# Optimization experiments

Hardware: AMD Instinct MI355X
Metric: run time of the kernel (lower is better)

The kernel has to match this reference:

```python
import jax, jax.numpy as jnp
from jax import lax
import numpy as np

N, K, QK, W = 10, 10, 150, 128
D = 256
HID = 100
CHANS = [1, 16, 32, 64, 128, 256]
STRIDES = [2, 2, 1, 1, 1]
ITERS = 3
BN_EPS = 1e-5


def setup_inputs() -> dict:
    key = jax.random.key(0)
    ks = jax.random.split(key, 12)
    inp = {
        "support": jax.random.normal(ks[0], (N, K, 1, W, W), jnp.float32),
        "query": jax.random.normal(ks[1], (QK, 1, W, W), jnp.float32),
    }
    for i in range(5):
        inp[f"conv_w{i}"] = jax.random.normal(ks[2 + i], (CHANS[i + 1], CHANS[i], 3, 3), jnp.float32) * 0.05
        inp[f"bn_g{i}"] = jnp.ones((CHANS[i + 1],), jnp.float32)
        inp[f"bn_b{i}"] = jnp.zeros((CHANS[i + 1],), jnp.float32)
    inp["trans_w"] = jax.random.normal(ks[8], (D, D), jnp.float32) * 0.05
    inp["trans_b"] = jnp.zeros((D,), jnp.float32)
    inp["bil_w"] = jax.random.normal(ks[9], (HID, D, D), jnp.float32) * 0.02
    inp["score_w"] = jax.random.normal(ks[10], (1, HID), jnp.float32) * 0.1
    inp["score_b"] = jnp.zeros((1,), jnp.float32)
    return inp


def _block(x, w, g, b, s):
    # Conv2d(k=3, pad=1, stride=s, no bias) -> BatchNorm(eval: mean=0, var=1) -> ReLU -> MaxPool2d(2)
    x = lax.conv_general_dilated(x, w, (s, s), ((1, 1), (1, 1)),
                                 dimension_numbers=('NCHW', 'OIHW', 'NCHW'))
    scale = (g / jnp.sqrt(1.0 + BN_EPS))[None, :, None, None]
    x = jax.nn.relu(x * scale + b[None, :, None, None])
    return lax.reduce_window(x, -jnp.inf, lax.max, (1, 1, 2, 2), (1, 1, 2, 2), 'VALID')


def reference(support, query,
              conv_w0, conv_w1, conv_w2, conv_w3, conv_w4,
              bn_g0, bn_g1, bn_g2, bn_g3, bn_g4,
              bn_b0, bn_b1, bn_b2, bn_b3, bn_b4,
              trans_w, trans_b, bil_w, score_w, score_b):
    n, k = support.shape[0], support.shape[1]
    qk = query.shape[0]
    w = support.shape[3]

    ws = [conv_w0, conv_w1, conv_w2, conv_w3, conv_w4]
    gs = [bn_g0, bn_g1, bn_g2, bn_g3, bn_g4]
    bs = [bn_b0, bn_b1, bn_b2, bn_b3, bn_b4]

    # run the conv backbone on support+query jointly (BN is per-sample in eval mode)
    x = jnp.concatenate([support.reshape(n * k, 1, w, w), query], axis=0)
    for cw, g, b, s in zip(ws, gs, bs, STRIDES):
        x = _block(x, cw, g, b, s)
    feats = x.reshape(x.shape[0], -1)              # (n*k + qk, 256); spatial is 1x1
    sup = feats[:n * k].reshape(n, k, -1)          # (n, k, d)
    q = feats[n * k:]                              # (qk, d)

    # dynamic routing: Transformer(e) is recomputed each iter on the same input -> hoist
    e = sup @ trans_w.T + trans_b                  # (n, k, d)
    b0 = jnp.zeros((n, k), sup.dtype)

    def step(bb, _):
        dcoef = jax.nn.softmax(bb, axis=1)[:, :, None]   # (n, k, 1)
        c = (dcoef * e).sum(axis=1)                      # (n, d)
        cn = jnp.sqrt((c * c).sum(axis=1, keepdims=True))
        c = c * (cn / (cn * cn + 1.0))                   # squash: ||c||^2/(||c||^2+1)/||c||
        db = (c[:, None, :] * e).sum(axis=2)             # (n, k)
        return bb + db, c

    _, cs = lax.scan(step, b0, None, length=ITERS)
    proto = cs[-1]                                  # (n, d)

    # NTN: bilinear score for every (query, proto) pair, exploiting the pair structure
    t1 = jnp.einsum('nc,hce->nhe', proto, bil_w)    # (n, HID, d)
    v = jnp.einsum('nhe,qe->qnh', t1, q)            # (qk, n, HID)
    s = jax.nn.relu(v) @ score_w[0] + score_b[0]    # (qk, n)
    return jax.nn.log_softmax(s, axis=1)
```

## Files before the change

### kernel.cpp

```cpp
#include <hip/hip_runtime.h>
#include <math.h>


#define BN_SCALE rsqrtf(1.0f + 1e-5f)

#define OFF_FEATS 0
#define OFF_E     64000
#define OFF_S     89600
#define OFF_T1    91136
#define OFF_PROTO 347136
#define OFF_W1T   349696
#define OFF_W2T   354304
#define OFF_W3T   372736
#define OFF_W4T   446464
#define OFF_TWT   741376
#define OFF_CNT   (OFF_S + 1500)

__global__ void k_prep(const float* __restrict__ w1, const float* __restrict__ w2,
                       const float* __restrict__ w3, const float* __restrict__ w4,
                       const float* __restrict__ tw, float* __restrict__ ws) {
  float* w1t = ws + OFF_W1T;
  float* w2t = ws + OFF_W2T;
  float* w3t = ws + OFF_W3T;
  float* w4t = ws + OFF_W4T;
  float* twt = ws + OFF_TWT;
  int i = blockIdx.x * 256 + threadIdx.x;
  if (i < 4608) {
    int oc = i & 31; int r = i >> 5; int tap = r % 9; int ic = r / 9;
    w1t[i] = w1[(oc * 16 + ic) * 9 + tap];
  } else if (i < 23040) {
    int j = i - 4608;
    int oc = j & 63; int r = j >> 6; int tap = r % 9; int ic = r / 9;
    w2t[j] = w2[(oc * 32 + ic) * 9 + tap];
  } else if (i < 96768) {
    int j = i - 23040;
    int oc = j & 127; int r = j >> 7; int tap = r % 9; int ic = r / 9;
    w3t[j] = w3[(oc * 64 + ic) * 9 + tap];
  } else if (i < 391680) {
    int j = i - 96768;
    int oc = j & 255; int r = j >> 8; int tap = r % 9; int ic = r / 9;
    w4t[j] = w4[(oc * 128 + ic) * 9 + tap];
  } else if (i < 457216) {
    int j = i - 391680;
    int d = j >> 8, c = j & 255;
    twt[j] = tw[c * 256 + d];
  } else if (i < 713216) {
    ws[OFF_T1 + (i - 457216)] = 0.f;
  } else if (i < 714717) {
    ws[OFF_S + (i - 713216)] = 0.f;
  }
}

__global__ void __launch_bounds__(1024, 4)
k_main(const float* __restrict__ sup, const float* __restrict__ qry,
       const float* __restrict__ w0, const float* __restrict__ g0, const float* __restrict__ b0,
       const float* __restrict__ g1, const float* __restrict__ b1,
       const float* __restrict__ g2, const float* __restrict__ b2,
       const float* __restrict__ g3, const float* __restrict__ b3,
       const float* __restrict__ g4, const float* __restrict__ b4,
       const float* __restrict__ tb, float* __restrict__ ws,
       float* __restrict__ feats_g, float* __restrict__ e_buf) {
  __shared__ float S[38404];
  const float* w1t = ws + OFF_W1T;
  const float* w2t = ws + OFF_W2T;
  const float* w3t = ws + OFF_W3T;
  const float* w4t = ws + OFF_W4T;
  const float* twt = ws + OFF_TWT;
  const int img = blockIdx.x;
  const int t = threadIdx.x;
  const int lane = t & 63, wid = t >> 6;
  float* sa1 = S;
  float* sa2 = S + 4096;
  float* sa3 = S + 7424;
  float* sft = S + 7936;
  float* a0p = S + 8580;
  float* RED = S + 8580;
  float* L1R = S + 28164;

  const float* in = (img < 100) ? (sup + (size_t)img * 16384)
                                : (qry + (size_t)(img - 100) * 16384);

  for (int i = t; i < 7424; i += 1024) S[i] = 0.f;
  for (int i = t; i < 19584; i += 1024) a0p[i] = 0.f;
  __syncthreads();

  {
    const int oc = wid;
    float wv[9];
#pragma unroll
    for (int k = 0; k < 9; k++) wv[k] = w0[oc * 9 + k];
    const float sc = g0[oc] * BN_SCALE, bs = b0[oc];
#pragma unroll 2
    for (int it2 = 0; it2 < 4; it2++) {
      const int s2 = it2 * 64 + lane;
      const int pr = s2 >> 3, pcq = s2 & 7;
      float acc[2][8];
#pragma unroll
      for (int j = 0; j < 8; j++) { acc[0][j] = 0.f; acc[1][j] = 0.f; }
#pragma unroll
      for (int d = 0; d < 5; d++) {
        const int ir = 4 * pr - 1 + d;
        float x[17];
        if (ir >= 0) {
          const float* rp = in + ir * 128 + 16 * pcq;
          float4 q0 = ((const float4*)rp)[0];
          float4 q1 = ((const float4*)rp)[1];
          float4 q2 = ((const float4*)rp)[2];
          float4 q3 = ((const float4*)rp)[3];
          x[0] = (pcq > 0) ? rp[-1] : 0.f;
          x[1] = q0.x;  x[2] = q0.y;  x[3] = q0.z;  x[4] = q0.w;
          x[5] = q1.x;  x[6] = q1.y;  x[7] = q1.z;  x[8] = q1.w;
          x[9] = q2.x;  x[10] = q2.y; x[11] = q2.z; x[12] = q2.w;
          x[13] = q3.x; x[14] = q3.y; x[15] = q3.z; x[16] = q3.w;
        } else {
#pragma unroll
          for (int k = 0; k < 17; k++) x[k] = 0.f;
        }
        if (d <= 2) {
          const int b9 = d * 3;
#pragma unroll
          for (int j = 0; j < 8; j++)
            acc[0][j] = fmaf(x[2 * j + 2], wv[b9 + 2],
                        fmaf(x[2 * j + 1], wv[b9 + 1],
                        fmaf(x[2 * j],     wv[b9],     acc[0][j])));
        }
        if (d >= 2) {
          const int b9 = (d - 2) * 3;
#pragma unroll
          for (int j = 0; j < 8; j++)
            acc[1][j] = fmaf(x[2 * j + 2], wv[b9 + 2],
                        fmaf(x[2 * j + 1], wv[b9 + 1],
                        fmaf(x[2 * j],     wv[b9],     acc[1][j])));
        }
      }
      float* op = a0p + oc * 1224 + (pr + 1) * 36 + 4 * pcq + 1;
#pragma unroll
      for (int p = 0; p < 4; p++) {
        float m = fmaf(acc[0][2 * p], sc, bs);
        m = fmaxf(m, fmaf(acc[0][2 * p + 1], sc, bs));
        m = fmaxf(m, fmaf(acc[1][2 * p], sc, bs));
        m = fmaxf(m, fmaf(acc[1][2 * p + 1], sc, bs));
        op[p] = fmaxf(m, 0.f);
      }
    }
  }
  __syncthreads();

  {
    const int pos = t & 63, py = pos >> 3, px = pos & 7;
    const int ocg = (t >> 6) & 7, icg = t >> 9;
    float acc[4][4];
#pragma unroll
    for (int j = 0; j < 4; j++)
#pragma unroll
      for (int p = 0; p < 4; p++) acc[j][p] = 0.f;
    for (int ii = 0; ii < 8; ii++) {
      const int ic = icg * 8 + ii;
      float4 wq[9];
#pragma unroll
      for (int k = 0; k < 9; k++)
        wq[k] = *(const float4*)(w1t + (ic * 9 + k) * 32 + 4 * ocg);
      float win[25];
      const float* bp = a0p + ic * 1224 + 4 * py * 36 + 4 * px;
#pragma unroll
      for (int d = 0; d < 5; d++) {
        float4 r4 = *(const float4*)(bp + d * 36);
        win[d * 5 + 0] = r4.x; win[d * 5 + 1] = r4.y;
        win[d * 5 + 2] = r4.z; win[d * 5 + 3] = r4.w;
        win[d * 5 + 4] = bp[d * 36 + 4];
      }
#pragma unroll
      for (int cy = 0; cy < 2; cy++)
#pragma unroll
        for (int cx = 0; cx < 2; cx++) {
          const int p = cy * 2 + cx;
#pragma unroll
          for (int ky = 0; ky < 3; ky++)
#pragma unroll
            for (int kx = 0; kx < 3; kx++) {
              const float iv = win[(2 * cy + ky) * 5 + (2 * cx + kx)];
              const float4 wk = wq[ky * 3 + kx];
              acc[0][p] = fmaf(iv, wk.x, acc[0][p]);
              acc[1][p] = fmaf(iv, wk.y, acc[1][p]);
              acc[2][p] = fmaf(iv, wk.z, acc[2][p]);
              acc[3][p] = fmaf(iv, wk.w, acc[3][p]);
            }
        }
    }
    const int slot = pos * 8 + ocg;
    if (icg == 1) {
      float* wp2 = L1R + slot * 20;
#pragma unroll
      for (int j = 0; j < 4; j++)
        *(float4*)(wp2 + j * 4) = make_float4(acc[j][0], acc[j][1], acc[j][2], acc[j][3]);
    }
    __syncthreads();
    if (icg == 0) {
      const float* rp2 = L1R + slot * 20;
#pragma unroll
      for (int j = 0; j < 4; j++) {
        float4 o = *(const float4*)(rp2 + j * 4);
        const int oc = ocg * 4 + j;
        const float sc = g1[oc] * BN_SCALE, bsj = b1[oc];
        float m = fmaf(acc[j][0] + o.x, sc, bsj);
        m = fmaxf(m, fmaf(acc[j][1] + o.y, sc, bsj));
        m = fmaxf(m, fmaf(acc[j][2] + o.z, sc, bsj));
        m = fmaxf(m, fmaf(acc[j][3] + o.w, sc, bsj));
        sa1[oc * 124 + (py + 1) * 12 + (px + 1)] = fmaxf(m, 0.f);
      }
    }
  }
  __syncthreads();

  {
    int oc = t & 63, icg = (t >> 6) & 3, pg = t >> 8;
    int pgy = pg >> 1, pgx = pg & 1;
    float acc[16];
#pragma unroll
    for (int p = 0; p < 16; p++) acc[p] = 0.f;
    float wc[9];
    {
      const float* wp = w2t + (icg * 8) * 576 + oc;
#pragma unroll
      for (int k = 0; k < 9; k++) wc[k] = wp[k * 64];
    }
    for (int ii = 0; ii < 8; ii++) {
      int ic = icg * 8 + ii;
      float wn[9];
      if (ii < 7) {
        const float* wp = w2t + (ic + 1) * 576 + oc;
#pragma unroll
        for (int k = 0; k < 9; k++) wn[k] = wp[k * 64];
      }
      float win[6][6];
      const float* bp = sa1 + ic * 124 + 4 * pgy * 12 + 4 * pgx;
#pragma unroll
      for (int d = 0; d < 6; d++) {
        float4 u = *(const float4*)(bp + d * 12);
        float2 v = *(const float2*)(bp + d * 12 + 4);
        win[d][0] = u.x; win[d][1] = u.y; win[d][2] = u.z; win[d][3] = u.w;
        win[d][4] = v.x; win[d][5] = v.y;
      }
#pragma unroll
      for (int u = 0; u < 4; u++)
#pragma unroll
        for (int v = 0; v < 4; v++) {
          float c = acc[u * 4 + v];
#pragma unroll
          for (int ky = 0; ky < 3; ky++)
#pragma unroll
            for (int kx = 0; kx < 3; kx++)
              c = fmaf(win[u + ky][v + kx], wc[ky * 3 + kx], c);
          acc[u * 4 + v] = c;
        }
      if (ii < 7) {
#pragma unroll
        for (int k = 0; k < 9; k++) wc[k] = wn[k];
      }
    }
#pragma unroll
    for (int j = 0; j < 16; j++) RED[j * 1024 + icg * 256 + pg * 64 + oc] = acc[j];
  }
  __syncthreads();
  if (t < 256) {
    int oc = t & 63, pg = t >> 6;
    int pgy = pg >> 1, pgx = pg & 1;
    float sc = g2[oc] * BN_SCALE, bsj = b2[oc];
#pragma unroll
    for (int cy = 0; cy < 2; cy++)
#pragma unroll
      for (int cx = 0; cx < 2; cx++) {
        float m = -1e30f;
#pragma unroll
        for (int a = 0; a < 2; a++)
#pragma unroll
          for (int b = 0; b < 2; b++) {
            int j = (2 * cy + a) * 4 + (2 * cx + b);
            float v = RED[j * 1024 + pg * 64 + oc] + RED[j * 1024 + 256 + pg * 64 + oc]
                    + RED[j * 1024 + 512 + pg * 64 + oc] + RED[j * 1024 + 768 + pg * 64 + oc];
            m = fmaxf(m, fmaf(v, sc, bsj));
          }
        sa2[oc * 52 + (1 + 2 * pgy + cy) * 8 + (1 + 2 * pgx + cx)] = fmaxf(m, 0.f);
      }
  }
  __syncthreads();

  {
    int oc = t & 127, icg = t >> 7;
    float acc[16];
#pragma unroll
    for (int p = 0; p < 16; p++) acc[p] = 0.f;
    float wc[9];
    {
      const float* wp = w3t + (icg * 8) * 1152 + oc;
#pragma unroll
      for (int k = 0; k < 9; k++) wc[k] = wp[k * 128];
    }
    for (int ii = 0; ii < 8; ii++) {
      int ic = icg * 8 + ii;
      float wn[9];
      if (ii < 7) {
        const float* wp = w3t + (ic + 1) * 1152 + oc;
#pragma unroll
        for (int k = 0; k < 9; k++) wn[k] = wp[k * 128];
      }
      float win[6][6];
      const float* bp = sa2 + ic * 52;
#pragma unroll
      for (int d = 0; d < 6; d++) {
        float4 u = *(const float4*)(bp + d * 8);
        float2 v = *(const float2*)(bp + d * 8 + 4);
        win[d][0] = u.x; win[d][1] = u.y; win[d][2] = u.z; win[d][3] = u.w;
        win[d][4] = v.x; win[d][5] = v.y;
      }
#pragma unroll
      for (int u = 0; u < 4; u++)
#pragma unroll
        for (int v = 0; v < 4; v++) {
          float c = acc[u * 4 + v];
#pragma unroll
          for (int ky = 0; ky < 3; ky++)
#pragma unroll
            for (int kx = 0; kx < 3; kx++)
              c = fmaf(win[u + ky][v + kx], wc[ky * 3 + kx], c);
          acc[u * 4 + v] = c;
        }
      if (ii < 7) {
#pragma unroll
        for (int k = 0; k < 9; k++) wc[k] = wn[k];
      }
    }
#pragma unroll
    for (int j = 0; j < 16; j++) RED[j * 1024 + icg * 128 + oc] = acc[j];
  }
  __syncthreads();
  if (t < 512) {
    int oc = t & 127, pp = t >> 7;
    int py = pp >> 1, px = pp & 1;
    float sc = g3[oc] * BN_SCALE, bsj = b3[oc];
    float m = -1e30f;
#pragma unroll
    for (int a = 0; a < 2; a++)
#pragma unroll
      for (int b = 0; b < 2; b++) {
        int j = (2 * py + a) * 4 + (2 * px + b);
        float v = 0.f;
#pragma unroll
        for (int g = 0; g < 8; g++) v += RED[j * 1024 + g * 128 + oc];
        m = fmaxf(m, fmaf(v, sc, bsj));
      }
    sa3[oc * 4 + pp] = fmaxf(m, 0.f);
  }
  __syncthreads();

  {
    int oc = t & 255, icq = t >> 8;
    float acc[4] = {0.f, 0.f, 0.f, 0.f};
    float wc[9];
    {
      const float* wp = w4t + (icq * 32) * 2304 + oc;
#pragma unroll
      for (int k = 0; k < 9; k++) wc[k] = wp[k * 256];
    }
    for (int ii = 0; ii < 32; ii++) {
      int ic = icq * 32 + ii;
      float wn[9];
      if (ii < 31) {
        const float* wp = w4t + (ic + 1) * 2304 + oc;
#pragma unroll
        for (int k = 0; k < 9; k++) wn[k] = wp[k * 256];
      }
      float4 iv = *(const float4*)(sa3 + ic * 4);
#pragma unroll
      for (int py = 0; py < 2; py++)
#pragma unroll
        for (int px = 0; px < 2; px++) {
          float c = acc[py * 2 + px];
          c = fmaf(iv.x, wc[(1 - py) * 3 + (1 - px)], c);
          c = fmaf(iv.y, wc[(1 - py) * 3 + (2 - px)], c);
          c = fmaf(iv.z, wc[(2 - py) * 3 + (1 - px)], c);
          c = fmaf(iv.w, wc[(2 - py) * 3 + (2 - px)], c);
          acc[py * 2 + px] = c;
        }
      if (ii < 31) {
#pragma unroll
        for (int k = 0; k < 9; k++) wc[k] = wn[k];
      }
    }
    if (icq) {
#pragma unroll
      for (int p = 0; p < 4; p++) RED[((icq - 1) * 256 + oc) * 4 + p] = acc[p];
    }
    __syncthreads();
    if (icq == 0) {
      float sc = g4[oc] * BN_SCALE, bsj = b4[oc];
      float m = -1e30f;
#pragma unroll
      for (int p = 0; p < 4; p++) {
        float v = acc[p] + RED[oc * 4 + p] + RED[(256 + oc) * 4 + p] + RED[(512 + oc) * 4 + p];
        m = fmaxf(m, fmaf(v, sc, bsj));
      }
      float r = fmaxf(m, 0.f);
      sft[oc] = r;
      feats_g[(size_t)img * 256 + oc] = r;
    }
  }
  __syncthreads();

  if (img < 100) {
    int c = t & 255, dq = t >> 8;
    float acc = 0.f;
    float wv = twt[(dq * 64) * 256 + c];
#pragma unroll 4
    for (int ii = 0; ii < 64; ii++) {
      int d = dq * 64 + ii;
      float wnext = (ii < 63) ? twt[(d + 1) * 256 + c] : 0.f;
      acc = fmaf(sft[d], wv, acc);
      wv = wnext;
    }
    if (dq) RED[(dq - 1) * 256 + c] = acc;
    __syncthreads();
    if (dq == 0)
      e_buf[img * 256 + c] = acc + RED[c] + RED[256 + c] + RED[512 + c] + tb[c];
  }
}

__global__ void k_routing(const float* __restrict__ e, float* __restrict__ proto) {
  int n = blockIdx.x;
  __shared__ float sb[10], sdc[10], red[4], red2[40], sfc[1];
  int t = threadIdx.x;
  int lane = t & 63, wid = t >> 6;
  float ek[10];
#pragma unroll
  for (int k = 0; k < 10; k++) ek[k] = e[n * 2560 + k * 256 + t];
  if (t < 10) sb[t] = 0.f;
  __syncthreads();
  float cd = 0.f;
  for (int iter = 0; iter < 3; iter++) {
    if (t == 0) {
      float mx = sb[0];
      for (int k = 1; k < 10; k++) mx = fmaxf(mx, sb[k]);
      float sum = 0.f;
      for (int k = 0; k < 10; k++) { float ex = expf(sb[k] - mx); sdc[k] = ex; sum += ex; }
      float inv = 1.f / sum;
      for (int k = 0; k < 10; k++) sdc[k] *= inv;
    }
    __syncthreads();
    cd = 0.f;
#pragma unroll
    for (int k = 0; k < 10; k++) cd = fmaf(sdc[k], ek[k], cd);
    float ss = cd * cd;
#pragma unroll
    for (int off = 32; off > 0; off >>= 1) ss += __shfl_down(ss, off, 64);
    if (lane == 0) red[wid] = ss;
    __syncthreads();
    if (t == 0) {
      float tot = red[0] + red[1] + red[2] + red[3];
      sfc[0] = sqrtf(tot) / (tot + 1.f);
    }
    __syncthreads();
    cd *= sfc[0];
    float pr[10];
#pragma unroll
    for (int k = 0; k < 10; k++) pr[k] = cd * ek[k];
#pragma unroll
    for (int off = 32; off > 0; off >>= 1)
#pragma unroll
      for (int k = 0; k < 10; k++) pr[k] += __shfl_down(pr[k], off, 64);
    if (lane == 0)
#pragma unroll
      for (int k = 0; k < 10; k++) red2[k * 4 + wid] = pr[k];
    __syncthreads();
    if (t < 10) sb[t] += red2[t * 4] + red2[t * 4 + 1] + red2[t * 4 + 2] + red2[t * 4 + 3];
    __syncthreads();
  }
  proto[n * 256 + t] = cd;
}

__global__ void k_t1(const float* __restrict__ proto, const float* __restrict__ bw,
                     float* __restrict__ t1) {
  __shared__ float pt[384];
  const int b = blockIdx.x;
  const int h = b >> 3, c0 = (b & 7) * 32;
  const int t = threadIdx.x;
  for (int i = t; i < 320; i += 256) {
    int n = i >> 5, cl = i & 31;
    pt[cl * 12 + n] = proto[n * 256 + c0 + cl];
  }
  __syncthreads();
  float acc[10];
#pragma unroll
  for (int n = 0; n < 10; n++) acc[n] = 0.f;
  const float* wp = bw + (size_t)h * 65536 + (size_t)c0 * 256 + t;
#pragma unroll 8
  for (int cl = 0; cl < 32; cl++) {
    float wv = wp[(size_t)cl * 256];
    float4 p0 = *(const float4*)(pt + cl * 12);
    float4 p1 = *(const float4*)(pt + cl * 12 + 4);
    float2 p2 = *(const float2*)(pt + cl * 12 + 8);
    acc[0] = fmaf(p0.x, wv, acc[0]); acc[1] = fmaf(p0.y, wv, acc[1]);
    acc[2] = fmaf(p0.z, wv, acc[2]); acc[3] = fmaf(p0.w, wv, acc[3]);
    acc[4] = fmaf(p1.x, wv, acc[4]); acc[5] = fmaf(p1.y, wv, acc[5]);
    acc[6] = fmaf(p1.z, wv, acc[6]); acc[7] = fmaf(p1.w, wv, acc[7]);
    acc[8] = fmaf(p2.x, wv, acc[8]); acc[9] = fmaf(p2.y, wv, acc[9]);
  }
#pragma unroll
  for (int n = 0; n < 10; n++)
    atomicAdd(&t1[((size_t)n * 100 + h) * 256 + t], acc[n]);
}

__global__ void k_score(const float* __restrict__ t1, const float* __restrict__ qf,
                        const float* __restrict__ sw, const float* __restrict__ sbp,
                        float* __restrict__ s, unsigned* __restrict__ cnt,
                        float* __restrict__ out) {
  __shared__ float sq[256];
  __shared__ float vb[2000];
  __shared__ int lastFlag;
  const int q = blockIdx.x >> 1, hh = blockIdx.x & 1;
  const int t = threadIdx.x;
  const int sl = t & 3, quad = t >> 2;
  sq[t] = qf[q * 256 + t];
  __syncthreads();
  const float4* qr = (const float4*)sq;
#pragma unroll
  for (int j = 0; j < 8; j++) {
    int lr = quad + 64 * j;
    if (lr < 500) {
      int n = lr / 50, hl = lr % 50;
      const float4* row = (const float4*)(t1 + ((size_t)(n * 100 + hh * 50 + hl)) * 256);
      float acc = 0.f;
#pragma unroll
      for (int d = 0; d < 16; d++) {
        float4 a = row[d * 4 + sl];
        float4 b = qr[d * 4 + sl];
        acc += a.x * b.x + a.y * b.y + a.z * b.z + a.w * b.w;
      }
      vb[lr * 4 + sl] = acc;
    }
  }
  __syncthreads();
  if (t < 10) {
    float sum = 0.f;
    for (int hl = 0; hl < 50; hl++) {
      int lr = t * 50 + hl;
      float d = vb[lr * 4] + vb[lr * 4 + 1] + vb[lr * 4 + 2] + vb[lr * 4 + 3];
      sum = fmaf(fmaxf(d, 0.f), sw[hh * 50 + hl], sum);
    }
    atomicAdd(&s[q * 10 + t], sum);
    __threadfence();
  }
  __syncthreads();
  if (t == 0) {
    unsigned old = atomicAdd(cnt, 1u);
    lastFlag = (old == 299u);
  }
  __syncthreads();
  if (lastFlag && t < 150) {
    float sb0 = sbp[0];
    float v[10];
    float mx = -1e30f;
#pragma unroll
    for (int n = 0; n < 10; n++) {
      v[n] = atomicAdd(&s[t * 10 + n], 0.f) + sb0;
      mx = fmaxf(mx, v[n]);
    }
    float sum2 = 0.f;
#pragma unroll
    for (int n = 0; n < 10; n++) sum2 += expf(v[n] - mx);
    float lse = mx + logf(sum2);
#pragma unroll
    for (int n = 0; n < 10; n++) out[t * 10 + n] = v[n] - lse;
  }
}

extern "C" void kernel_launch(void* const* d_in, const int* in_sizes, int n_in,
                              void* d_out, int out_size, void* d_ws, size_t ws_size,
                              hipStream_t stream) {
  const float* support = (const float*)d_in[0];
  const float* query   = (const float*)d_in[1];
  const float* conv_w[5]; const float* bn_g[5]; const float* bn_b[5];
  for (int i = 0; i < 5; i++) {
    conv_w[i] = (const float*)d_in[2 + 3 * i];
    bn_g[i]   = (const float*)d_in[3 + 3 * i];
    bn_b[i]   = (const float*)d_in[4 + 3 * i];
  }
  const float* trans_w = (const float*)d_in[17];
  const float* trans_b = (const float*)d_in[18];
  const float* bil_w   = (const float*)d_in[19];
  const float* score_w = (const float*)d_in[20];
  const float* score_b = (const float*)d_in[21];
  float* out = (float*)d_out;
  float* ws = (float*)d_ws;

  float* feats = ws + OFF_FEATS;
  float* e_buf = ws + OFF_E;
  float* s_buf = ws + OFF_S;
  float* t1    = ws + OFF_T1;
  float* proto = ws + OFF_PROTO;
  unsigned* cnt = (unsigned*)(ws + OFF_CNT);

  k_prep<<<2793, 256, 0, stream>>>(conv_w[1], conv_w[2], conv_w[3], conv_w[4],
                                   trans_w, ws);
  k_main<<<250, 1024, 0, stream>>>(support, query,
                                   conv_w[0], bn_g[0], bn_b[0],
                                   bn_g[1], bn_b[1], bn_g[2], bn_b[2],
                                   bn_g[3], bn_b[3], bn_g[4], bn_b[4],
                                   trans_b, ws, feats, e_buf);
  k_routing<<<10, 256, 0, stream>>>(e_buf, proto);
  k_t1<<<800, 256, 0, stream>>>(proto, bil_w, t1);
  k_score<<<300, 256, 0, stream>>>(t1, feats + 100 * 256, score_w, score_b,
                                   s_buf, cnt, out);
}
```

Before: 224.2 us.

## Rework conv0 thread mapping, vectorize shared stores, split log-softmax into own kernel

Layer 0 now gives each warp two output channels over half the rows, so each input load is reused across two channels, and results go out as float4 shared stores. The padded layout shifts so the layer-1 window read becomes one scalar plus one aligned float4. The shared zero-init is merged into a single float4 loop, and the reduction slot order changes. The last-block atomic counter in k_score is replaced by a separate tiny log-softmax kernel, which adds a launch but removes the atomics and fences. The unroll factor in k_t1 also drops from 8 to 4.

```diff
diff --git a/kernel.cpp b/kernel.cpp
--- a/kernel.cpp
+++ b/kernel.cpp
@@ -14,7 +14,6 @@
 #define OFF_W3T   372736
 #define OFF_W4T   446464
 #define OFF_TWT   741376
-#define OFF_CNT   (OFF_S + 1500)
 
 __global__ void k_prep(const float* __restrict__ w1, const float* __restrict__ w2,
                        const float* __restrict__ w3, const float* __restrict__ w4,
@@ -46,7 +45,7 @@
     twt[j] = tw[c * 256 + d];
   } else if (i < 713216) {
     ws[OFF_T1 + (i - 457216)] = 0.f;
-  } else if (i < 714717) {
+  } else if (i < 714716) {
     ws[OFF_S + (i - 713216)] = 0.f;
   }
 }
@@ -60,7 +59,7 @@
        const float* __restrict__ g4, const float* __restrict__ b4,
        const float* __restrict__ tb, float* __restrict__ ws,
        float* __restrict__ feats_g, float* __restrict__ e_buf) {
-  __shared__ float S[38404];
+  __shared__ __align__(16) float S[38404];
   const float* w1t = ws + OFF_W1T;
   const float* w2t = ws + OFF_W2T;
   const float* w3t = ws + OFF_W3T;
@@ -80,23 +79,31 @@
   const float* in = (img < 100) ? (sup + (size_t)img * 16384)
                                 : (qry + (size_t)(img - 100) * 16384);
 
-  for (int i = t; i < 7424; i += 1024) S[i] = 0.f;
-  for (int i = t; i < 19584; i += 1024) a0p[i] = 0.f;
-  __syncthreads();
-
   {
-    const int oc = wid;
-    float wv[9];
-#pragma unroll
-    for (int k = 0; k < 9; k++) wv[k] = w0[oc * 9 + k];
-    const float sc = g0[oc] * BN_SCALE, bs = b0[oc];
-#pragma unroll 2
-    for (int it2 = 0; it2 < 4; it2++) {
-      const int s2 = it2 * 64 + lane;
+    float4* S4 = (float4*)S;
+    const float4 z4 = make_float4(0.f, 0.f, 0.f, 0.f);
+    for (int i = t; i < 7041; i += 1024) S4[i] = z4;
+  }
+  __syncthreads();
+
+  {
+    const int ocp = wid & 7;
+    const int rhalf = wid >> 3;
+    const int oc0 = 2 * ocp, oc1 = oc0 + 1;
+    float wv0[9], wv1[9];
+#pragma unroll
+    for (int k = 0; k < 9; k++) { wv0[k] = w0[oc0 * 9 + k]; wv1[k] = w0[oc1 * 9 + k]; }
+    const float sc0 = g0[oc0] * BN_SCALE, bs0 = b0[oc0];
+    const float sc1 = g0[oc1] * BN_SCALE, bs1 = b0[oc1];
+#pragma unroll
+    for (int it2 = 0; it2 < 2; it2++) {
+      const int s2 = rhalf * 128 + it2 * 64 + lane;
       const int pr = s2 >> 3, pcq = s2 & 7;
-      float acc[2][8];
-#pragma unroll
-      for (int j = 0; j < 8; j++) { acc[0][j] = 0.f; acc[1][j] = 0.f; }
+      float ac0[2][8], ac1[2][8];
+#pragma unroll
+      for (int j = 0; j < 8; j++) {
+        ac0[0][j] = 0.f; ac0[1][j] = 0.f; ac1[0][j] = 0.f; ac1[1][j] = 0.f;
+      }
 #pragma unroll
       for (int d = 0; d < 5; d++) {
         const int ir = 4 * pr - 1 + d;
@@ -119,28 +126,50 @@
         if (d <= 2) {
           const int b9 = d * 3;
 #pragma unroll
-          for (int j = 0; j < 8; j++)
-            acc[0][j] = fmaf(x[2 * j + 2], wv[b9 + 2],
-                        fmaf(x[2 * j + 1], wv[b9 + 1],
-                        fmaf(x[2 * j],     wv[b9],     acc[0][j])));
+          for (int j = 0; j < 8; j++) {
+            ac0[0][j] = fmaf(x[2 * j + 2], wv0[b9 + 2],
+                        fmaf(x[2 * j + 1], wv0[b9 + 1],
+                        fmaf(x[2 * j],     wv0[b9],     ac0[0][j])));
+            ac1[0][j] = fmaf(x[2 * j + 2], wv1[b9 + 2],
+                        fmaf(x[2 * j + 1], wv1[b9 + 1],
+                        fmaf(x[2 * j],     wv1[b9],     ac1[0][j])));
+          }
         }
         if (d >= 2) {
           const int b9 = (d - 2) * 3;
 #pragma unroll
-          for (int j = 0; j < 8; j++)
-            acc[1][j] = fmaf(x[2 * j + 2], wv[b9 + 2],
-                        fmaf(x[2 * j + 1], wv[b9 + 1],
-                        fmaf(x[2 * j],     wv[b9],     acc[1][j])));
-        }
-      }
-      float* op = a0p + oc * 1224 + (pr + 1) * 36 + 4 * pcq + 1;
-#pragma unroll
-      for (int p = 0; p < 4; p++) {
-        float m = fmaf(acc[0][2 * p], sc, bs);
-        m = fmaxf(m, fmaf(acc[0][2 * p + 1], sc, bs));
-        m = fmaxf(m, fmaf(acc[1][2 * p], sc, bs));
-        m = fmaxf(m, fmaf(acc[1][2 * p + 1], sc, bs));
-        op[p] = fmaxf(m, 0.f);
+          for (int j = 0; j < 8; j++) {
+            ac0[1][j] = fmaf(x[2 * j + 2], wv0[b9 + 2],
+                        fmaf(x[2 * j + 1], wv0[b9 + 1],
+                        fmaf(x[2 * j],     wv0[b9],     ac0[1][j])));
+            ac1[1][j] = fmaf(x[2 * j + 2], wv1[b9 + 2],
+                        fmaf(x[2 * j + 1], wv1[b9 + 1],
+                        fmaf(x[2 * j],     wv1[b9],     ac1[1][j])));
+          }
+        }
+      }
+      {
+        float v[4];
+#pragma unroll
+        for (int p = 0; p < 4; p++) {
+          float m = fmaf(ac0[0][2 * p], sc0, bs0);
+          m = fmaxf(m, fmaf(ac0[0][2 * p + 1], sc0, bs0));
+          m = fmaxf(m, fmaf(ac0[1][2 * p], sc0, bs0));
+          m = fmaxf(m, fmaf(ac0[1][2 * p + 1], sc0, bs0));
+          v[p] = fmaxf(m, 0.f);
+        }
+        *(float4*)(a0p + oc0 * 1224 + (pr + 1) * 36 + 4 * pcq) =
+            make_float4(v[0], v[1], v[2], v[3]);
+#pragma unroll
+        for (int p = 0; p < 4; p++) {
+          float m = fmaf(ac1[0][2 * p], sc1, bs1);
+          m = fmaxf(m, fmaf(ac1[0][2 * p + 1], sc1, bs1));
+          m = fmaxf(m, fmaf(ac1[1][2 * p], sc1, bs1));
+          m = fmaxf(m, fmaf(ac1[1][2 * p + 1], sc1, bs1));
+          v[p] = fmaxf(m, 0.f);
+        }
+        *(float4*)(a0p + oc1 * 1224 + (pr + 1) * 36 + 4 * pcq) =
+            make_float4(v[0], v[1], v[2], v[3]);
       }
     }
   }
@@ -154,20 +183,22 @@
     for (int j = 0; j < 4; j++)
 #pragma unroll
       for (int p = 0; p < 4; p++) acc[j][p] = 0.f;
+    const int ic0 = icg * 8;
     for (int ii = 0; ii < 8; ii++) {
-      const int ic = icg * 8 + ii;
+      const int ic = ic0 + ii;
       float4 wq[9];
 #pragma unroll
       for (int k = 0; k < 9; k++)
         wq[k] = *(const float4*)(w1t + (ic * 9 + k) * 32 + 4 * ocg);
       float win[25];
-      const float* bp = a0p + ic * 1224 + 4 * py * 36 + 4 * px;
+      const float* rb = a0p + ic * 1224 + 4 * py * 36 + 4 * px;
 #pragma unroll
       for (int d = 0; d < 5; d++) {
-        float4 r4 = *(const float4*)(bp + d * 36);
-        win[d * 5 + 0] = r4.x; win[d * 5 + 1] = r4.y;
-        win[d * 5 + 2] = r4.z; win[d * 5 + 3] = r4.w;
-        win[d * 5 + 4] = bp[d * 36 + 4];
+        const float* rp = rb + d * 36;
+        win[d * 5 + 0] = rp[-1];
+        float4 r4 = *(const float4*)rp;
+        win[d * 5 + 1] = r4.x; win[d * 5 + 2] = r4.y;
+        win[d * 5 + 3] = r4.z; win[d * 5 + 4] = r4.w;
       }
 #pragma unroll
       for (int cy = 0; cy < 2; cy++)
@@ -187,7 +218,7 @@
             }
         }
     }
-    const int slot = pos * 8 + ocg;
+    const int slot = ocg * 64 + pos;
     if (icg == 1) {
       float* wp2 = L1R + slot * 20;
 #pragma unroll
@@ -492,7 +523,7 @@
 #pragma unroll
   for (int n = 0; n < 10; n++) acc[n] = 0.f;
   const float* wp = bw + (size_t)h * 65536 + (size_t)c0 * 256 + t;
-#pragma unroll 8
+#pragma unroll 4
   for (int cl = 0; cl < 32; cl++) {
     float wv = wp[(size_t)cl * 256];
     float4 p0 = *(const float4*)(pt + cl * 12);
@@ -510,12 +541,9 @@
 }
 
 __global__ void k_score(const float* __restrict__ t1, const float* __restrict__ qf,
-                        const float* __restrict__ sw, const float* __restrict__ sbp,
-                        float* __restrict__ s, unsigned* __restrict__ cnt,
-                        float* __restrict__ out) {
+                        const float* __restrict__ sw, float* __restrict__ s) {
   __shared__ float sq[256];
   __shared__ float vb[2000];
-  __shared__ int lastFlag;
   const int q = blockIdx.x >> 1, hh = blockIdx.x & 1;
   const int t = threadIdx.x;
   const int sl = t & 3, quad = t >> 2;
@@ -547,30 +575,27 @@
       sum = fmaf(fmaxf(d, 0.f), sw[hh * 50 + hl], sum);
     }
     atomicAdd(&s[q * 10 + t], sum);
-    __threadfence();
-  }
-  __syncthreads();
-  if (t == 0) {
-    unsigned old = atomicAdd(cnt, 1u);
-    lastFlag = (old == 299u);
-  }
-  __syncthreads();
-  if (lastFlag && t < 150) {
-    float sb0 = sbp[0];
-    float v[10];
-    float mx = -1e30f;
-#pragma unroll
-    for (int n = 0; n < 10; n++) {
-      v[n] = atomicAdd(&s[t * 10 + n], 0.f) + sb0;
-      mx = fmaxf(mx, v[n]);
-    }
-    float sum2 = 0.f;
-#pragma unroll
-    for (int n = 0; n < 10; n++) sum2 += expf(v[n] - mx);
-    float lse = mx + logf(sum2);
-#pragma unroll
-    for (int n = 0; n < 10; n++) out[t * 10 + n] = v[n] - lse;
-  }
+  }
+}
+
+__global__ void k_lsm(const float* __restrict__ s, const float* __restrict__ sbp,
+                      float* __restrict__ out) {
+  int q = threadIdx.x;
+  if (q >= 150) return;
+  float sb0 = sbp[0];
+  float v[10];
+  float mx = -1e30f;
+#pragma unroll
+  for (int n = 0; n < 10; n++) {
+    v[n] = s[q * 10 + n] + sb0;
+    mx = fmaxf(mx, v[n]);
+  }
+  float sum = 0.f;
+#pragma unroll
+  for (int n = 0; n < 10; n++) sum += expf(v[n] - mx);
+  float lse = mx + logf(sum);
+#pragma unroll
+  for (int n = 0; n < 10; n++) out[q * 10 + n] = v[n] - lse;
 }
 
 extern "C" void kernel_launch(void* const* d_in, const int* in_sizes, int n_in,
@@ -597,7 +622,6 @@
   float* s_buf = ws + OFF_S;
   float* t1    = ws + OFF_T1;
   float* proto = ws + OFF_PROTO;
-  unsigned* cnt = (unsigned*)(ws + OFF_CNT);
 
   k_prep<<<2793, 256, 0, stream>>>(conv_w[1], conv_w[2], conv_w[3], conv_w[4],
                                    trans_w, ws);
@@ -608,6 +632,6 @@
                                    trans_b, ws, feats, e_buf);
   k_routing<<<10, 256, 0, stream>>>(e_buf, proto);
   k_t1<<<800, 256, 0, stream>>>(proto, bil_w, t1);
-  k_score<<<300, 256, 0, stream>>>(t1, feats + 100 * 256, score_w, score_b,
-                                   s_buf, cnt, out);
+  k_score<<<300, 256, 0, stream>>>(t1, feats + 100 * 256, score_w, s_buf);
+  k_lsm<<<1, 256, 0, stream>>>(s_buf, score_b, out);
 }
```

Result: faster. 210.4 us (-6.2%).
